# Kernel optimization log

Measured on AMD Instinct MI355X. Metric: run time of the kernel, lower is better.

Reference implementation:

```python
import jax
import jax.numpy as jnp
from jax import lax
import numpy as np

B, H, W, C = 8, 128, 128, 64
KH, KW = 3, 3
K = KH * KW
OUT = 64
PAD = 1  # 'same' padding for 3x3, stride 1, dilation 1


def setup_inputs() -> dict:
    key = jax.random.key(0)
    k1, k2, k3, k4 = jax.random.split(key, 4)
    scale = 0.05  # keep learned offsets in a sane pixel range
    x = jax.random.normal(k1, (B, H, W, C), dtype=jnp.float32)
    offset_kernel = jax.random.normal(k2, (KH, KW, C, 2 * K), dtype=jnp.float32) * scale
    mask_kernel = jax.random.normal(k3, (KH, KW, C, K), dtype=jnp.float32) * scale
    filt = jax.random.normal(k4, (OUT, C, KH, KW), dtype=jnp.float32) * scale
    return {"x": x, "offset_kernel": offset_kernel, "mask_kernel": mask_kernel, "filt": filt}


def _conv_same(x, kernel):
    # x: [B,H,W,C], kernel: [kh,kw,Cin,Cout] -> [B,H,W,Cout]
    return lax.conv_general_dilated(
        x, kernel, window_strides=(1, 1), padding='SAME',
        dimension_numbers=('NHWC', 'HWIO', 'NHWC'))


def _bilinear_gather(img, py, px):
    # img: [B,C,H,W]; py,px: [B,K,H,W] float sampling coords (zero outside image)
    b, c, h, w = img.shape
    imf = img.reshape(b, c, h * w)
    y0 = jnp.floor(py)
    x0 = jnp.floor(px)
    ly = py - y0
    lx = px - x0

    def corner(yi, xi, wgt):
        valid = (yi >= 0) & (yi <= h - 1) & (xi >= 0) & (xi <= w - 1)
        yc = jnp.clip(yi, 0, h - 1).astype(jnp.int32)
        xc = jnp.clip(xi, 0, w - 1).astype(jnp.int32)
        idx = yc * w + xc  # [B,K,H,W]
        v = jax.vmap(lambda im, ix: jnp.take(im, ix, axis=1))(imf, idx)  # [B,C,K,H,W]
        return v * (wgt * valid.astype(img.dtype))[:, None]

    return (corner(y0, x0, (1 - ly) * (1 - lx))
            + corner(y0, x0 + 1, (1 - ly) * lx)
            + corner(y0 + 1, x0, ly * (1 - lx))
            + corner(y0 + 1, x0 + 1, ly * lx))


def reference(x, offset_kernel, mask_kernel, filt):
    # offset conv and mask conv (mask goes through sigmoid), both channels_last
    offset = _conv_same(x, offset_kernel)                 # [B,H,W,2K]
    mask = jax.nn.sigmoid(_conv_same(x, mask_kernel))     # [B,H,W,K]

    xc = jnp.transpose(x, (0, 3, 1, 2))                   # [B,C,H,W]
    off = jnp.transpose(offset, (0, 3, 1, 2)).reshape(B, K, 2, H, W)
    dy, dx = off[:, :, 0], off[:, :, 1]                   # [B,K,H,W]
    m = jnp.transpose(mask, (0, 3, 1, 2))                 # [B,K,H,W]

    # base sampling grid: p = out_loc + kernel_offset - pad + learned offset
    hh = jnp.arange(H, dtype=jnp.float32)
    ww = jnp.arange(W, dtype=jnp.float32)
    ky = jnp.repeat(jnp.arange(KH, dtype=jnp.float32), KW)  # [K]
    kx = jnp.tile(jnp.arange(KW, dtype=jnp.float32), KH)    # [K]
    py = hh[None, None, :, None] + (ky - PAD)[None, :, None, None] + dy  # [B,K,H,W]
    px = ww[None, None, None, :] + (kx - PAD)[None, :, None, None] + dx

    cols = _bilinear_gather(xc, py, px)                   # [B,C,K,H,W]
    cols = cols * m[:, None]                              # modulated (offset_groups=1)

    fk = filt.reshape(OUT, C, K)
    out = jnp.einsum('bcknm,ock->bonm', cols, fk)         # [B,OUT,H,W]
    return jnp.transpose(out, (0, 2, 3, 1))               # NHWC, bias disabled
```

## Files before the change

kernel.cpp:

```cpp
#include <hip/hip_runtime.h>
#include <hip/hip_fp16.h>
#include <math.h>

#define BB 8
#define HH 128
#define WW 128
#define CC 64
#define KK 9
#define OUTC 64
#define TW 16
#define KTOT 576
#define NELEM (BB*HH*WW*CC)
#define XSW 3456

typedef __attribute__((ext_vector_type(8))) _Float16 half8v;
typedef __attribute__((ext_vector_type(4))) float float4v;

static __device__ __forceinline__ unsigned short f2h(float f) {
    return __half_as_ushort(__float2half(f));
}
static __device__ __forceinline__ unsigned h2bits(float f) {
    __half2 h = __float2half2_rn(f);
    unsigned r; __builtin_memcpy(&r, &h, 4); return r;
}
static __device__ __forceinline__ __half2 bits2h(unsigned w) {
    __half2 h; __builtin_memcpy(&h, &w, 4); return h;
}

static __device__ __forceinline__ int frag_addr(int p, int kappa) {
    int chunk = kappa >> 3;
    return ((chunk >> 2) << 9) + ((chunk & 3) << 7) + ((p ^ (chunk & 7)) << 3) + (kappa & 7);
}

__global__ __launch_bounds__(256) void prep_all(
    const float* __restrict__ x, const float* __restrict__ offk,
    const float* __restrict__ mk, const float* __restrict__ filt,
    unsigned short* __restrict__ fbf,
    unsigned short* __restrict__ wcf,
    unsigned short* __restrict__ xf,
    int do_x)
{
    int bid = blockIdx.x, tid = threadIdx.x;
    if (bid < 144) {
        int j = bid * 256 + tid;
        {
            int w = j / 9216, rem = j - w * 9216;
            int ks = rem >> 9, ln = (rem >> 3) & 63, sj = rem & 7;
            int pl = ln & 15, lg = ln >> 4;
            int o = w * 16 + pl, kap = ks * 32 + lg * 8 + sj;
            int k = kap >> 6, c = kap & 63;
            fbf[j] = f2h(filt[(o * CC + c) * KK + k]);
        }
        if (j < 18432) {
            int nh = j / 9216, rem = j - nh * 9216;
            int ks = rem >> 9, ln = (rem >> 3) & 63, sj = rem & 7;
            int pl = ln & 15, lg = ln >> 4;
            int o = nh * 16 + pl, kap = ks * 32 + lg * 8 + sj;
            int k = kap >> 6, c = kap & 63;
            float v = 0.f;
            if (o < 18)      v = offk[(k * CC + c) * 18 + o];
            else if (o < 27) v = mk[(k * CC + c) * 9 + (o - 18)];
            wcf[j] = f2h(v);
        }
        return;
    }
    if (!do_x) return;
    int i = (bid - 144) * 256 + tid;
    const float* src = x + (size_t)i * 8;
    float4 a = *(const float4*)(src);
    float4 c = *(const float4*)(src + 4);
    float v[8] = {a.x, a.y, a.z, a.w, c.x, c.y, c.z, c.w};
    unsigned q[4];
#pragma unroll
    for (int j = 0; j < 4; ++j)
        q[j] = (unsigned)f2h(v[2 * j]) | ((unsigned)f2h(v[2 * j + 1]) << 16);
    *(uint4*)(xf + (size_t)i * 8) = make_uint4(q[0], q[1], q[2], q[3]);
}

template<int HASB>
__global__ __launch_bounds__(256, 7) void deform_conv_fused(
    const float* __restrict__ x,
    const unsigned short* __restrict__ xf,
    const unsigned short* __restrict__ fbf,
    const unsigned short* __restrict__ wcf,
    float* __restrict__ out)
{
    __shared__ __align__(16) unsigned short ims[TW * KTOT];
    __shared__ __align__(16) union UU {
        float ps2[4][TW][18];
        struct { int4 c[144]; uint4 w[144]; } gs;
    } u;

    const int tid  = threadIdx.x;
    const int lane = tid & 63;
    const int wave = tid >> 6;
    const int pl = lane & 15;
    const int lg = lane >> 4;
    const int off_e = lg * 128 + ((pl ^ lg) << 3);
    const int off_o = lg * 128 + ((pl ^ (lg + 4)) << 3);

    const int swz = (blockIdx.x & 7) * 1024 + (blockIdx.x >> 3);
    const int bw = swz & 7;
    const int h  = (swz >> 3) & 127;
    const int b  = swz >> 10;
    const int w0 = bw * TW;

#pragma unroll
    for (int it = 0; it < 2; ++it) {
        int e = tid + it * 256;
        if (it == 1 && e >= 432) break;
        int r    = (e >= 288) ? 2 : (e >= 144) ? 1 : 0;
        int rem2 = e - r * 144;
        int px   = rem2 >> 3;
        int c8   = rem2 & 7;
        int y = h + r - 1, xg = w0 + px - 1;
        int lidx = (r * 18 + px) * 64 + ((c8 * 8) ^ ((px & 7) << 3));
        uint4 val = make_uint4(0u, 0u, 0u, 0u);
        if ((unsigned)y < (unsigned)HH && (unsigned)xg < (unsigned)WW) {
            int goff = ((b * HH + y) * WW + xg) * CC + c8 * 8;
            if (HASB) {
                val = *(const uint4*)(xf + goff);
            } else {
                float4 v0 = *(const float4*)(x + goff);
                float4 v1 = *(const float4*)(x + goff + 4);
                float vv[8] = {v0.x, v0.y, v0.z, v0.w, v1.x, v1.y, v1.z, v1.w};
                unsigned q[4];
#pragma unroll
                for (int j = 0; j < 4; ++j)
                    q[j] = (unsigned)f2h(vv[2 * j]) | ((unsigned)f2h(vv[2 * j + 1]) << 16);
                val = make_uint4(q[0], q[1], q[2], q[3]);
            }
        }
        *(uint4*)(ims + lidx) = val;
    }
    __syncthreads();

    const int nh = wave & 1, kh = wave >> 1;
    float4v acc = {0.f, 0.f, 0.f, 0.f};
    __builtin_amdgcn_s_setprio(1);
#pragma unroll
    for (int ks9 = 0; ks9 < 9; ++ks9) {
        const int ksg = kh * 9 + ks9;
        const int tap = ksg >> 1;
        const int cb  = (ksg & 1) * 32 + lg * 8;
        const int ky = tap / 3, kx = tap - ky * 3;
        const int px = pl + kx;
        const int base = (ky * 18 + px) * 64 + (cb ^ ((px & 7) << 3));
        half8v af = *(const half8v*)(ims + base);
        half8v bv = *(const half8v*)(wcf + ((nh * 18 + ksg) << 9) + (lane << 3));
        acc = __builtin_amdgcn_mfma_f32_16x16x32_f16(af, bv, acc, 0, 0, 0);
    }
    __builtin_amdgcn_s_setprio(0);
#pragma unroll
    for (int r = 0; r < 4; ++r)
        u.ps2[wave][lg * 4 + r][pl] = acc[r];

    const unsigned short* Bpf = fbf + ((wave * 18) << 9) + (lane << 3);
    half8v bp0 = *(const half8v*)(Bpf);
    half8v bp1 = *(const half8v*)(Bpf + 512);
    __syncthreads();

    const int sp = tid / 9, sk = tid - (tid / 9) * 9;
    float s_dy = 0.f, s_dx = 0.f, s_ml = 0.f;
    if (tid < 144) {
        auto rd = [&](int o) {
            int nhh = o >> 4, col = o & 15;
            return u.ps2[nhh][sp][col] + u.ps2[2 + nhh][sp][col];
        };
        s_dy = rd(2 * sk); s_dx = rd(2 * sk + 1); s_ml = rd(18 + sk);
    }
    __syncthreads();

    if (tid < 144) {
        float m  = 1.f / (1.f + __expf(-s_ml));
        float py = (float)(h + (sk / 3) - 1) + s_dy;
        float px = (float)(w0 + sp + (sk % 3) - 1) + s_dx;
        float y0 = floorf(py), x0 = floorf(px);
        float ly = py - y0, lx = px - x0;
        bool vy0 = (y0 >= 0.f)  && (y0 <= 127.f);
        bool vy1 = (y0 >= -1.f) && (y0 <= 126.f);
        bool vx0 = (x0 >= 0.f)  && (x0 <= 127.f);
        bool vx1 = (x0 >= -1.f) && (x0 <= 126.f);
        float wy0 = 1.f - ly, wx0 = 1.f - lx;
        int iy0 = (int)fminf(fmaxf(y0, 0.f), 127.f);
        int iy1 = (int)fminf(fmaxf(y0 + 1.f, 0.f), 127.f);
        int ix0 = (int)fminf(fmaxf(x0, 0.f), 127.f);
        int ix1 = (int)fminf(fmaxf(x0 + 1.f, 0.f), 127.f);
        int base = b * (HH * WW * CC);
        u.gs.c[tid] = make_int4(base + (iy0 * WW + ix0) * CC,
                                base + (iy0 * WW + ix1) * CC,
                                base + (iy1 * WW + ix0) * CC,
                                base + (iy1 * WW + ix1) * CC);
        u.gs.w[tid] = make_uint4(h2bits((vy0 && vx0) ? wy0 * wx0 * m : 0.f),
                                 h2bits((vy0 && vx1) ? wy0 * lx  * m : 0.f),
                                 h2bits((vy1 && vx0) ? ly  * wx0 * m : 0.f),
                                 h2bits((vy1 && vx1) ? ly  * lx  * m : 0.f));
    }
    __syncthreads();

    if (HASB) {
        for (int t = tid; t < 1152; t += 256) {
            int pair = t >> 3, c8 = t & 7;
            int p = pair / 9, k = pair - (pair / 9) * 9;
            int4  cc = u.gs.c[pair];
            uint4 wq = u.gs.w[pair];
            __half2 w0 = bits2h(wq.x), w1 = bits2h(wq.y);
            __half2 w2 = bits2h(wq.z), w3 = bits2h(wq.w);
            int co = c8 * 8;
            uint4 u00 = *(const uint4*)(xf + cc.x + co);
            uint4 u01 = *(const uint4*)(xf + cc.y + co);
            uint4 u10 = *(const uint4*)(xf + cc.z + co);
            uint4 u11 = *(const uint4*)(xf + cc.w + co);
            const unsigned* a00 = (const unsigned*)&u00;
            const unsigned* a01 = (const unsigned*)&u01;
            const unsigned* a10 = (const unsigned*)&u10;
            const unsigned* a11 = (const unsigned*)&u11;
            unsigned qq[4];
#pragma unroll
            for (int jj = 0; jj < 4; ++jj) {
                __half2 acc2 = __hmul2(bits2h(a00[jj]), w0);
                acc2 = __hfma2(bits2h(a01[jj]), w1, acc2);
                acc2 = __hfma2(bits2h(a10[jj]), w2, acc2);
                acc2 = __hfma2(bits2h(a11[jj]), w3, acc2);
                __builtin_memcpy(&qq[jj], &acc2, 4);
            }
            *(uint4*)(ims + frag_addr(p, k * 64 + co)) = make_uint4(qq[0], qq[1], qq[2], qq[3]);
        }
    } else {
        for (int t = tid; t < 1152; t += 256) {
            int pair = t >> 3, c8 = t & 7;
            int p = pair / 9, k = pair - (pair / 9) * 9;
            int4  cc = u.gs.c[pair];
            uint4 wq = u.gs.w[pair];
            float wx = __half2float(bits2h(wq.x).x);
            float wy = __half2float(bits2h(wq.y).x);
            float wz = __half2float(bits2h(wq.z).x);
            float ww = __half2float(bits2h(wq.w).x);
            int co = c8 * 8;
            float r[8];
#pragma unroll
            for (int half = 0; half < 2; ++half) {
                float4 v00 = *(const float4*)(x + cc.x + co + half * 4);
                float4 v01 = *(const float4*)(x + cc.y + co + half * 4);
                float4 v10 = *(const float4*)(x + cc.z + co + half * 4);
                float4 v11 = *(const float4*)(x + cc.w + co + half * 4);
                r[half * 4 + 0] = wx * v00.x + wy * v01.x + wz * v10.x + ww * v11.x;
                r[half * 4 + 1] = wx * v00.y + wy * v01.y + wz * v10.y + ww * v11.y;
                r[half * 4 + 2] = wx * v00.z + wy * v01.z + wz * v10.z + ww * v11.z;
                r[half * 4 + 3] = wx * v00.w + wy * v01.w + wz * v10.w + ww * v11.w;
            }
            unsigned qq[4];
#pragma unroll
            for (int jj = 0; jj < 4; ++jj)
                qq[jj] = (unsigned)f2h(r[2 * jj]) | ((unsigned)f2h(r[2 * jj + 1]) << 16);
            *(uint4*)(ims + frag_addr(p, k * 64 + co)) = make_uint4(qq[0], qq[1], qq[2], qq[3]);
        }
    }
    __syncthreads();

    {
        float4v accA = {0.f, 0.f, 0.f, 0.f}, accB = {0.f, 0.f, 0.f, 0.f};
        __builtin_amdgcn_s_setprio(1);
#pragma unroll
        for (int ks = 0; ks < 18; ++ks) {
            half8v a  = *(const half8v*)(ims + ks * 512 + ((ks & 1) ? off_o : off_e));
            half8v bv = (ks == 0) ? bp0 : (ks == 1) ? bp1
                      : *(const half8v*)(Bpf + (ks << 9));
            if (ks & 1) accB = __builtin_amdgcn_mfma_f32_16x16x32_f16(a, bv, accB, 0, 0, 0);
            else        accA = __builtin_amdgcn_mfma_f32_16x16x32_f16(a, bv, accA, 0, 0, 0);
        }
        __builtin_amdgcn_s_setprio(0);
        const int o = wave * 16 + pl;
        const size_t rowbase = (size_t)(b * HH + h) * WW + w0;
#pragma unroll
        for (int r = 0; r < 4; ++r) {
            int p = lg * 4 + r;
            out[(rowbase + p) * OUTC + o] = accA[r] + accB[r];
        }
    }
}

extern "C" void kernel_launch(void* const* d_in, const int* in_sizes, int n_in,
                              void* d_out, int out_size, void* d_ws, size_t ws_size,
                              hipStream_t stream) {
    const float* x    = (const float*)d_in[0];
    const float* offk = (const float*)d_in[1];
    const float* mk   = (const float*)d_in[2];
    const float* filt = (const float*)d_in[3];
    float* out = (float*)d_out;
    unsigned short* fbf = (unsigned short*)d_ws;
    unsigned short* wcf = fbf + OUTC * KTOT;
    unsigned short* xf  = wcf + 32 * KTOT;
    size_t need = (size_t)(OUTC + 32) * KTOT * 2 + (size_t)NELEM * 2;
    int do_x = (ws_size >= need) ? 1 : 0;
    prep_all<<<144 + (do_x ? 4096 : 0), 256, 0, stream>>>(x, offk, mk, filt, fbf, wcf, xf, do_x);
    if (do_x)
        deform_conv_fused<1><<<BB * HH * (WW / TW), 256, 0, stream>>>(x, xf, fbf, wcf, out);
    else
        deform_conv_fused<0><<<BB * HH * (WW / TW), 256, 0, stream>>>(x, xf, fbf, wcf, out);
}
```

Before: 65.72 us.

## Split fused deformable conv into offset-setup and gather-GEMM kernels

Splits the single fused kernel into two. The first computes the offset/mask conv and writes compact per-pair sampling metadata to global memory: a base address with two edge flags and four fp16 weights. The second kernel loads that metadata up front, gathers the bilinear samples and runs the output GEMM. The aim is to lower per-block shared memory and register pressure and shorten each block's serial dependency chain, at the cost of an extra launch and a global round trip for about 12 bytes per pair. It also drops the s_setprio hints in the fallback kernel and packs the corner addresses into one word.

After: 77.62 us. 1.18x slower.

```diff
diff --git a/kernel.cpp b/kernel.cpp
--- a/kernel.cpp
+++ b/kernel.cpp
@@ -11,17 +11,13 @@
 #define TW 16
 #define KTOT 576
 #define NELEM (BB*HH*WW*CC)
-#define XSW 3456
+#define NPAIR (BB*HH*WW*KK)
 
 typedef __attribute__((ext_vector_type(8))) _Float16 half8v;
 typedef __attribute__((ext_vector_type(4))) float float4v;
 
 static __device__ __forceinline__ unsigned short f2h(float f) {
     return __half_as_ushort(__float2half(f));
-}
-static __device__ __forceinline__ unsigned h2bits(float f) {
-    __half2 h = __float2half2_rn(f);
-    unsigned r; __builtin_memcpy(&r, &h, 4); return r;
 }
 static __device__ __forceinline__ __half2 bits2h(unsigned w) {
     __half2 h; __builtin_memcpy(&h, &w, 4); return h;
@@ -77,6 +73,199 @@
     *(uint4*)(xf + (size_t)i * 8) = make_uint4(q[0], q[1], q[2], q[3]);
 }
 
+__global__ __launch_bounds__(256, 8) void conv_setup(
+    const unsigned short* __restrict__ xf,
+    const unsigned short* __restrict__ wcf,
+    unsigned* __restrict__ gsa,
+    uint2* __restrict__ gsw)
+{
+    __shared__ __align__(16) unsigned short tile[3 * 18 * 64];
+    __shared__ float ps2[4][TW][18];
+
+    const int tid  = threadIdx.x;
+    const int lane = tid & 63;
+    const int wave = tid >> 6;
+    const int pl = lane & 15;
+    const int lg = lane >> 4;
+
+    const int swz = (blockIdx.x & 7) * 1024 + (blockIdx.x >> 3);
+    const int bw = swz & 7;
+    const int h  = (swz >> 3) & 127;
+    const int b  = swz >> 10;
+    const int w0 = bw * TW;
+
+#pragma unroll
+    for (int it = 0; it < 2; ++it) {
+        int e = tid + it * 256;
+        if (it == 1 && tid >= 176) break;
+        int r    = (e >= 288) ? 2 : (e >= 144) ? 1 : 0;
+        int rem2 = e - r * 144;
+        int px   = rem2 >> 3;
+        int c8   = rem2 & 7;
+        int y = h + r - 1, xg = w0 + px - 1;
+        int lidx = (r * 18 + px) * 64 + ((c8 * 8) ^ ((px & 7) << 3));
+        uint4 val = make_uint4(0u, 0u, 0u, 0u);
+        if ((unsigned)y < (unsigned)HH && (unsigned)xg < (unsigned)WW)
+            val = *(const uint4*)(xf + ((b * HH + y) * WW + xg) * CC + c8 * 8);
+        *(uint4*)(tile + lidx) = val;
+    }
+    __syncthreads();
+
+    const int nh = wave & 1, kh = wave >> 1;
+    float4v acc = {0.f, 0.f, 0.f, 0.f};
+    __builtin_amdgcn_s_setprio(1);
+#pragma unroll
+    for (int ks9 = 0; ks9 < 9; ++ks9) {
+        const int ksg = kh * 9 + ks9;
+        const int tap = ksg >> 1;
+        const int cb  = (ksg & 1) * 32 + lg * 8;
+        const int ky = tap / 3, kx = tap - ky * 3;
+        const int px = pl + kx;
+        const int base = (ky * 18 + px) * 64 + (cb ^ ((px & 7) << 3));
+        half8v af = *(const half8v*)(tile + base);
+        half8v bv = *(const half8v*)(wcf + ((nh * 18 + ksg) << 9) + (lane << 3));
+        acc = __builtin_amdgcn_mfma_f32_16x16x32_f16(af, bv, acc, 0, 0, 0);
+    }
+    __builtin_amdgcn_s_setprio(0);
+#pragma unroll
+    for (int r = 0; r < 4; ++r)
+        ps2[wave][lg * 4 + r][pl] = acc[r];
+    __syncthreads();
+
+    if (tid < 144) {
+        const int sp = tid / 9, sk = tid - (tid / 9) * 9;
+        auto rd = [&](int o) {
+            int nhh = o >> 4, col = o & 15;
+            return ps2[nhh][sp][col] + ps2[2 + nhh][sp][col];
+        };
+        float s_dy = rd(2 * sk), s_dx = rd(2 * sk + 1), s_ml = rd(18 + sk);
+        float m  = 1.f / (1.f + __expf(-s_ml));
+        float py = (float)(h + (sk / 3) - 1) + s_dy;
+        float px = (float)(w0 + sp + (sk % 3) - 1) + s_dx;
+        float y0 = floorf(py), x0 = floorf(px);
+        float ly = py - y0, lx = px - x0;
+        bool vy0 = (y0 >= 0.f)  && (y0 <= 127.f);
+        bool vy1 = (y0 >= -1.f) && (y0 <= 126.f);
+        bool vx0 = (x0 >= 0.f)  && (x0 <= 127.f);
+        bool vx1 = (x0 >= -1.f) && (x0 <= 126.f);
+        float wy0 = 1.f - ly, wx0 = 1.f - lx;
+        int iy0 = (int)fminf(fmaxf(y0, 0.f), 127.f);
+        int ix0 = (int)fminf(fmaxf(x0, 0.f), 127.f);
+        bool fy = (y0 >= 0.f) && (y0 <= 126.f);
+        bool fx = (x0 >= 0.f) && (x0 <= 126.f);
+        int cc00 = b * (HH * WW * CC) + (iy0 * WW + ix0) * CC;
+        unsigned meta = (unsigned)cc00 | (fx ? (1u << 30) : 0u) | (fy ? (1u << 31) : 0u);
+        float w0v = (vy0 && vx0) ? wy0 * wx0 * m : 0.f;
+        float w1v = (vy0 && vx1) ? wy0 * lx  * m : 0.f;
+        float w2v = (vy1 && vx0) ? ly  * wx0 * m : 0.f;
+        float w3v = (vy1 && vx1) ? ly  * lx  * m : 0.f;
+        unsigned w01 = (unsigned)f2h(w0v) | ((unsigned)f2h(w1v) << 16);
+        unsigned w23 = (unsigned)f2h(w2v) | ((unsigned)f2h(w3v) << 16);
+        int gp = ((b * HH + h) * WW + w0) * KK + tid;
+        gsa[gp] = meta;
+        gsw[gp] = make_uint2(w01, w23);
+    }
+}
+
+__global__ __launch_bounds__(256, 7) void gather_gemm(
+    const unsigned short* __restrict__ xf,
+    const unsigned* __restrict__ gsa,
+    const uint2* __restrict__ gsw,
+    const unsigned short* __restrict__ fbf,
+    float* __restrict__ out)
+{
+    __shared__ __align__(16) unsigned short ims[TW * KTOT];
+
+    const int tid  = threadIdx.x;
+    const int lane = tid & 63;
+    const int wave = tid >> 6;
+    const int pl = lane & 15;
+    const int lg = lane >> 4;
+    const int off_e = lg * 128 + ((pl ^ lg) << 3);
+    const int off_o = lg * 128 + ((pl ^ (lg + 4)) << 3);
+
+    const int swz = (blockIdx.x & 7) * 1024 + (blockIdx.x >> 3);
+    const int bw = swz & 7;
+    const int h  = (swz >> 3) & 127;
+    const int b  = swz >> 10;
+    const int w0 = bw * TW;
+
+    const unsigned short* Bpf = fbf + ((wave * 18) << 9) + (lane << 3);
+    half8v bp0 = *(const half8v*)(Bpf);
+    half8v bp1 = *(const half8v*)(Bpf + 512);
+
+    const int gbase = ((b * HH + h) * WW + w0) * KK;
+    const int c8 = tid & 7, co = c8 * 8;
+    const int pr = tid >> 3;
+    const int pr4 = (pr + 128 < 144) ? pr + 128 : 143;
+    uint  m0 = gsa[gbase + pr];       uint2 q0 = gsw[gbase + pr];
+    uint  m1 = gsa[gbase + pr + 32];  uint2 q1 = gsw[gbase + pr + 32];
+    uint  m2 = gsa[gbase + pr + 64];  uint2 q2 = gsw[gbase + pr + 64];
+    uint  m3 = gsa[gbase + pr + 96];  uint2 q3 = gsw[gbase + pr + 96];
+    uint  m4 = gsa[gbase + pr4];      uint2 q4 = gsw[gbase + pr4];
+
+    auto gtask = [&](uint m, uint2 q, int pair) {
+        int pp = (pair * 57) >> 9;
+        int kk = pair - pp * 9;
+        int c00 = (int)(m & 0x00FFFFFFu) + co;
+        int dxo = (m & (1u << 30)) ? CC : 0;
+        int dyo = (m & (1u << 31)) ? WW * CC : 0;
+        int c01 = c00 + dxo;
+        int c10 = c00 + dyo;
+        int c11 = c01 + dyo;
+        uint4 u00 = *(const uint4*)(xf + c00);
+        uint4 u01 = *(const uint4*)(xf + c01);
+        uint4 u10 = *(const uint4*)(xf + c10);
+        uint4 u11 = *(const uint4*)(xf + c11);
+        __half2 wv0 = __half2half2(__ushort_as_half((unsigned short)(q.x & 0xFFFF)));
+        __half2 wv1 = __half2half2(__ushort_as_half((unsigned short)(q.x >> 16)));
+        __half2 wv2 = __half2half2(__ushort_as_half((unsigned short)(q.y & 0xFFFF)));
+        __half2 wv3 = __half2half2(__ushort_as_half((unsigned short)(q.y >> 16)));
+        const unsigned* a00 = (const unsigned*)&u00;
+        const unsigned* a01 = (const unsigned*)&u01;
+        const unsigned* a10 = (const unsigned*)&u10;
+        const unsigned* a11 = (const unsigned*)&u11;
+        unsigned qq[4];
+#pragma unroll
+        for (int jj = 0; jj < 4; ++jj) {
+            __half2 acc2 = __hmul2(bits2h(a00[jj]), wv0);
+            acc2 = __hfma2(bits2h(a01[jj]), wv1, acc2);
+            acc2 = __hfma2(bits2h(a10[jj]), wv2, acc2);
+            acc2 = __hfma2(bits2h(a11[jj]), wv3, acc2);
+            __builtin_memcpy(&qq[jj], &acc2, 4);
+        }
+        *(uint4*)(ims + frag_addr(pp, kk * 64 + co)) = make_uint4(qq[0], qq[1], qq[2], qq[3]);
+    };
+
+    gtask(m0, q0, pr);
+    gtask(m1, q1, pr + 32);
+    gtask(m2, q2, pr + 64);
+    gtask(m3, q3, pr + 96);
+    if (tid < 128) gtask(m4, q4, pr + 128);
+    __syncthreads();
+
+    {
+        float4v accA = {0.f, 0.f, 0.f, 0.f}, accB = {0.f, 0.f, 0.f, 0.f};
+        __builtin_amdgcn_s_setprio(1);
+#pragma unroll
+        for (int ks = 0; ks < 18; ++ks) {
+            half8v a  = *(const half8v*)(ims + ks * 512 + ((ks & 1) ? off_o : off_e));
+            half8v bv = (ks == 0) ? bp0 : (ks == 1) ? bp1
+                      : *(const half8v*)(Bpf + (ks << 9));
+            if (ks & 1) accB = __builtin_amdgcn_mfma_f32_16x16x32_f16(a, bv, accB, 0, 0, 0);
+            else        accA = __builtin_amdgcn_mfma_f32_16x16x32_f16(a, bv, accA, 0, 0, 0);
+        }
+        __builtin_amdgcn_s_setprio(0);
+        const int o = wave * 16 + pl;
+        const size_t rowbase = (size_t)(b * HH + h) * WW + w0;
+#pragma unroll
+        for (int r = 0; r < 4; ++r) {
+            int p = lg * 4 + r;
+            out[(rowbase + p) * OUTC + o] = accA[r] + accB[r];
+        }
+    }
+}
+
 template<int HASB>
 __global__ __launch_bounds__(256, 7) void deform_conv_fused(
     const float* __restrict__ x,
@@ -108,7 +297,7 @@
 #pragma unroll
     for (int it = 0; it < 2; ++it) {
         int e = tid + it * 256;
-        if (it == 1 && e >= 432) break;
+        if (it == 1 && tid >= 176) break;
         int r    = (e >= 288) ? 2 : (e >= 144) ? 1 : 0;
         int rem2 = e - r * 144;
         int px   = rem2 >> 3;
@@ -137,7 +326,6 @@
 
     const int nh = wave & 1, kh = wave >> 1;
     float4v acc = {0.f, 0.f, 0.f, 0.f};
-    __builtin_amdgcn_s_setprio(1);
 #pragma unroll
     for (int ks9 = 0; ks9 < 9; ++ks9) {
         const int ksg = kh * 9 + ks9;
@@ -150,7 +338,6 @@
         half8v bv = *(const half8v*)(wcf + ((nh * 18 + ksg) << 9) + (lane << 3));
         acc = __builtin_amdgcn_mfma_f32_16x16x32_f16(af, bv, acc, 0, 0, 0);
     }
-    __builtin_amdgcn_s_setprio(0);
 #pragma unroll
     for (int r = 0; r < 4; ++r)
         u.ps2[wave][lg * 4 + r][pl] = acc[r];
@@ -191,22 +378,24 @@
                                 base + (iy0 * WW + ix1) * CC,
                                 base + (iy1 * WW + ix0) * CC,
                                 base + (iy1 * WW + ix1) * CC);
-        u.gs.w[tid] = make_uint4(h2bits((vy0 && vx0) ? wy0 * wx0 * m : 0.f),
-                                 h2bits((vy0 && vx1) ? wy0 * lx  * m : 0.f),
-                                 h2bits((vy1 && vx0) ? ly  * wx0 * m : 0.f),
-                                 h2bits((vy1 && vx1) ? ly  * lx  * m : 0.f));
-    }
-    __syncthreads();
-
-    if (HASB) {
-        for (int t = tid; t < 1152; t += 256) {
-            int pair = t >> 3, c8 = t & 7;
-            int p = pair / 9, k = pair - (pair / 9) * 9;
-            int4  cc = u.gs.c[pair];
-            uint4 wq = u.gs.w[pair];
-            __half2 w0 = bits2h(wq.x), w1 = bits2h(wq.y);
-            __half2 w2 = bits2h(wq.z), w3 = bits2h(wq.w);
-            int co = c8 * 8;
+        auto h2b = [](float f) { __half2 hh = __float2half2_rn(f);
+                                 unsigned r; __builtin_memcpy(&r, &hh, 4); return r; };
+        u.gs.w[tid] = make_uint4(h2b((vy0 && vx0) ? wy0 * wx0 * m : 0.f),
+                                 h2b((vy0 && vx1) ? wy0 * lx  * m : 0.f),
+                                 h2b((vy1 && vx0) ? ly  * wx0 * m : 0.f),
+                                 h2b((vy1 && vx1) ? ly  * lx  * m : 0.f));
+    }
+    __syncthreads();
+
+    for (int t = tid; t < 1152; t += 256) {
+        int pair = t >> 3, c8 = t & 7;
+        int p = pair / 9, k = pair - (pair / 9) * 9;
+        int4  cc = u.gs.c[pair];
+        uint4 wq = u.gs.w[pair];
+        int co = c8 * 8;
+        if (HASB) {
+            __half2 wv0 = bits2h(wq.x), wv1 = bits2h(wq.y);
+            __half2 wv2 = bits2h(wq.z), wv3 = bits2h(wq.w);
             uint4 u00 = *(const uint4*)(xf + cc.x + co);
             uint4 u01 = *(const uint4*)(xf + cc.y + co);
             uint4 u10 = *(const uint4*)(xf + cc.z + co);
@@ -218,25 +407,18 @@
             unsigned qq[4];
 #pragma unroll
             for (int jj = 0; jj < 4; ++jj) {
-                __half2 acc2 = __hmul2(bits2h(a00[jj]), w0);
-                acc2 = __hfma2(bits2h(a01[jj]), w1, acc2);
-                acc2 = __hfma2(bits2h(a10[jj]), w2, acc2);
-                acc2 = __hfma2(bits2h(a11[jj]), w3, acc2);
+                __half2 acc2 = __hmul2(bits2h(a00[jj]), wv0);
+                acc2 = __hfma2(bits2h(a01[jj]), wv1, acc2);
+                acc2 = __hfma2(bits2h(a10[jj]), wv2, acc2);
+                acc2 = __hfma2(bits2h(a11[jj]), wv3, acc2);
                 __builtin_memcpy(&qq[jj], &acc2, 4);
             }
             *(uint4*)(ims + frag_addr(p, k * 64 + co)) = make_uint4(qq[0], qq[1], qq[2], qq[3]);
-        }
-    } else {
-        for (int t = tid; t < 1152; t += 256) {
-            int pair = t >> 3, c8 = t & 7;
-            int p = pair / 9, k = pair - (pair / 9) * 9;
-            int4  cc = u.gs.c[pair];
-            uint4 wq = u.gs.w[pair];
+        } else {
             float wx = __half2float(bits2h(wq.x).x);
             float wy = __half2float(bits2h(wq.y).x);
             float wz = __half2float(bits2h(wq.z).x);
             float ww = __half2float(bits2h(wq.w).x);
-            int co = c8 * 8;
             float r[8];
 #pragma unroll
             for (int half = 0; half < 2; ++half) {
@@ -260,7 +442,6 @@
 
     {
         float4v accA = {0.f, 0.f, 0.f, 0.f}, accB = {0.f, 0.f, 0.f, 0.f};
-        __builtin_amdgcn_s_setprio(1);
 #pragma unroll
         for (int ks = 0; ks < 18; ++ks) {
             half8v a  = *(const half8v*)(ims + ks * 512 + ((ks & 1) ? off_o : off_e));
@@ -269,7 +450,6 @@
             if (ks & 1) accB = __builtin_amdgcn_mfma_f32_16x16x32_f16(a, bv, accB, 0, 0, 0);
             else        accA = __builtin_amdgcn_mfma_f32_16x16x32_f16(a, bv, accA, 0, 0, 0);
         }
-        __builtin_amdgcn_s_setprio(0);
         const int o = wave * 16 + pl;
         const size_t rowbase = (size_t)(b * HH + h) * WW + w0;
 #pragma unroll
@@ -291,11 +471,18 @@
     unsigned short* fbf = (unsigned short*)d_ws;
     unsigned short* wcf = fbf + OUTC * KTOT;
     unsigned short* xf  = wcf + 32 * KTOT;
-    size_t need = (size_t)(OUTC + 32) * KTOT * 2 + (size_t)NELEM * 2;
-    int do_x = (ws_size >= need) ? 1 : 0;
-    prep_all<<<144 + (do_x ? 4096 : 0), 256, 0, stream>>>(x, offk, mk, filt, fbf, wcf, xf, do_x);
-    if (do_x)
-        deform_conv_fused<1><<<BB * HH * (WW / TW), 256, 0, stream>>>(x, xf, fbf, wcf, out);
-    else
-        deform_conv_fused<0><<<BB * HH * (WW / TW), 256, 0, stream>>>(x, xf, fbf, wcf, out);
-}
+    unsigned* gsa = (unsigned*)(xf + NELEM);
+    uint2* gsw = (uint2*)(gsa + NPAIR);
+    size_t need = (size_t)(OUTC + 32) * KTOT * 2 + (size_t)NELEM * 2
+                + (size_t)NPAIR * 4 + (size_t)NPAIR * 8;
+    int do_split = (ws_size >= need) ? 1 : 0;
+    prep_all<<<144 + (do_split ? 4096 : 0), 256, 0, stream>>>(
+        x, offk, mk, filt, fbf, wcf, xf, do_split);
+    if (do_split) {
+        conv_setup<<<BB * HH * (WW / TW), 256, 0, stream>>>(xf, wcf, gsa, gsw);
+        gather_gemm<<<BB * HH * (WW / TW), 256, 0, stream>>>(xf, gsa, gsw, fbf, out);
+    } else {
+        deform_conv_fused<0><<<BB * HH * (WW / TW), 256, 0, stream>>>(
+            x, nullptr, fbf, wcf, out);
+    }
+}
```

## Software-pipeline bilinear gather loads with inline asm and explicit vmcnt waits

Applied to the files above, without the earlier changes.

Replaces the strided gather loop in the fp16 path with a manually unrolled, double-buffered sequence. Each thread issues the next pair's four global_load_dwordx4 through inline asm before doing the half2 blend for the current pair, and waits with explicit s_waitcnt vmcnt. This aims to keep more memory requests in flight and hide gather latency. The cost is more registers, so launch bounds drop from 7 to 6 blocks per CU; the last round is predicated and reuses clamped pair indices for threads that have no work.

Result: no change. 66.35 us (+1.0%).

```diff
diff --git a/kernel.cpp b/kernel.cpp
--- a/kernel.cpp
+++ b/kernel.cpp
@@ -11,10 +11,10 @@
 #define TW 16
 #define KTOT 576
 #define NELEM (BB*HH*WW*CC)
-#define XSW 3456
 
 typedef __attribute__((ext_vector_type(8))) _Float16 half8v;
 typedef __attribute__((ext_vector_type(4))) float float4v;
+typedef __attribute__((ext_vector_type(4))) unsigned uint4v;
 
 static __device__ __forceinline__ unsigned short f2h(float f) {
     return __half_as_ushort(__float2half(f));
@@ -26,6 +26,13 @@
 static __device__ __forceinline__ __half2 bits2h(unsigned w) {
     __half2 h; __builtin_memcpy(&h, &w, 4); return h;
 }
+
+static __device__ __forceinline__ void gload(uint4v& d, const unsigned short* p) {
+    asm volatile("global_load_dwordx4 %0, %1, off" : "=&v"(d) : "v"(p));
+}
+#define VWAIT(N)                                                     \
+    asm volatile("s_waitcnt vmcnt(" #N ")" ::: "memory");            \
+    __builtin_amdgcn_sched_barrier(0)
 
 static __device__ __forceinline__ int frag_addr(int p, int kappa) {
     int chunk = kappa >> 3;
@@ -78,7 +85,7 @@
 }
 
 template<int HASB>
-__global__ __launch_bounds__(256, 7) void deform_conv_fused(
+__global__ __launch_bounds__(256, 6) void deform_conv_fused(
     const float* __restrict__ x,
     const unsigned short* __restrict__ xf,
     const unsigned short* __restrict__ fbf,
@@ -108,7 +115,7 @@
 #pragma unroll
     for (int it = 0; it < 2; ++it) {
         int e = tid + it * 256;
-        if (it == 1 && e >= 432) break;
+        if (it == 1 && tid >= 176) break;
         int r    = (e >= 288) ? 2 : (e >= 144) ? 1 : 0;
         int rem2 = e - r * 144;
         int px   = rem2 >> 3;
@@ -198,34 +205,60 @@
     }
     __syncthreads();
 
+    const int cog = (tid & 7) * 8;
+    const int prg = tid >> 3;
+
     if (HASB) {
-        for (int t = tid; t < 1152; t += 256) {
-            int pair = t >> 3, c8 = t & 7;
-            int p = pair / 9, k = pair - (pair / 9) * 9;
-            int4  cc = u.gs.c[pair];
-            uint4 wq = u.gs.w[pair];
-            __half2 w0 = bits2h(wq.x), w1 = bits2h(wq.y);
-            __half2 w2 = bits2h(wq.z), w3 = bits2h(wq.w);
-            int co = c8 * 8;
-            uint4 u00 = *(const uint4*)(xf + cc.x + co);
-            uint4 u01 = *(const uint4*)(xf + cc.y + co);
-            uint4 u10 = *(const uint4*)(xf + cc.z + co);
-            uint4 u11 = *(const uint4*)(xf + cc.w + co);
-            const unsigned* a00 = (const unsigned*)&u00;
-            const unsigned* a01 = (const unsigned*)&u01;
-            const unsigned* a10 = (const unsigned*)&u10;
-            const unsigned* a11 = (const unsigned*)&u11;
+        uint4v a0, a1, a2, a3, b0, b1, b2, b3;
+        int4  cc;
+        uint4 wqa, wqb;
+        const int p4 = (tid < 128) ? prg + 128 : prg;
+
+        auto gmath = [&](const uint4v& s0, const uint4v& s1,
+                         const uint4v& s2, const uint4v& s3,
+                         uint4 wq, int pair, bool pred) {
+            int pp = pair / 9, kk = pair - (pair / 9) * 9;
+            __half2 wv0 = bits2h(wq.x), wv1 = bits2h(wq.y);
+            __half2 wv2 = bits2h(wq.z), wv3 = bits2h(wq.w);
             unsigned qq[4];
 #pragma unroll
             for (int jj = 0; jj < 4; ++jj) {
-                __half2 acc2 = __hmul2(bits2h(a00[jj]), w0);
-                acc2 = __hfma2(bits2h(a01[jj]), w1, acc2);
-                acc2 = __hfma2(bits2h(a10[jj]), w2, acc2);
-                acc2 = __hfma2(bits2h(a11[jj]), w3, acc2);
+                __half2 acc2 = __hmul2(bits2h(s0[jj]), wv0);
+                acc2 = __hfma2(bits2h(s1[jj]), wv1, acc2);
+                acc2 = __hfma2(bits2h(s2[jj]), wv2, acc2);
+                acc2 = __hfma2(bits2h(s3[jj]), wv3, acc2);
                 __builtin_memcpy(&qq[jj], &acc2, 4);
             }
-            *(uint4*)(ims + frag_addr(p, k * 64 + co)) = make_uint4(qq[0], qq[1], qq[2], qq[3]);
-        }
+            if (pred)
+                *(uint4*)(ims + frag_addr(pp, kk * 64 + cog)) =
+                    make_uint4(qq[0], qq[1], qq[2], qq[3]);
+        };
+
+        cc = u.gs.c[prg];       wqa = u.gs.w[prg];
+        gload(a0, xf + cc.x + cog); gload(a1, xf + cc.y + cog);
+        gload(a2, xf + cc.z + cog); gload(a3, xf + cc.w + cog);
+        cc = u.gs.c[prg + 32];  wqb = u.gs.w[prg + 32];
+        gload(b0, xf + cc.x + cog); gload(b1, xf + cc.y + cog);
+        gload(b2, xf + cc.z + cog); gload(b3, xf + cc.w + cog);
+        VWAIT(4);
+        gmath(a0, a1, a2, a3, wqa, prg, true);
+        cc = u.gs.c[prg + 64];  wqa = u.gs.w[prg + 64];
+        gload(a0, xf + cc.x + cog); gload(a1, xf + cc.y + cog);
+        gload(a2, xf + cc.z + cog); gload(a3, xf + cc.w + cog);
+        VWAIT(4);
+        gmath(b0, b1, b2, b3, wqb, prg + 32, true);
+        cc = u.gs.c[prg + 96];  wqb = u.gs.w[prg + 96];
+        gload(b0, xf + cc.x + cog); gload(b1, xf + cc.y + cog);
+        gload(b2, xf + cc.z + cog); gload(b3, xf + cc.w + cog);
+        VWAIT(4);
+        gmath(a0, a1, a2, a3, wqa, prg + 64, true);
+        cc = u.gs.c[p4];        wqa = u.gs.w[p4];
+        gload(a0, xf + cc.x + cog); gload(a1, xf + cc.y + cog);
+        gload(a2, xf + cc.z + cog); gload(a3, xf + cc.w + cog);
+        VWAIT(4);
+        gmath(b0, b1, b2, b3, wqb, prg + 96, true);
+        VWAIT(0);
+        gmath(a0, a1, a2, a3, wqa, p4, tid < 128);
     } else {
         for (int t = tid; t < 1152; t += 256) {
             int pair = t >> 3, c8 = t & 7;
```
